# Performance work log

Hardware: AMD Instinct MI355X
Metric: run time of the kernel (lower is better)

Reference implementation:

```python
import jax, jax.numpy as jnp
import numpy as np

B, M, HS, K = 2, 2048, 1024, 16
D = HS // K


def setup_inputs() -> dict:
    key = jax.random.key(0)
    k1, k2, k3, k4 = jax.random.split(key, 4)
    s = 1.0 / np.sqrt(HS)
    return {
        "h": jax.random.normal(k1, (B, M, HS), jnp.float32),
        "W_span": jax.random.normal(k2, (2 * K, HS), jnp.float32) * s,
        "W_val": jax.random.normal(k3, (HS, HS), jnp.float32) * s,
        "W_out": jax.random.normal(k4, (HS, HS), jnp.float32) * s,
    }


def _head_reshape(x, d):
    # (B, M, K*d) -> (B*K, M, d), matching torch view/transpose in head_reshape
    b, m, _ = x.shape
    return x.reshape(b, m, K, d).transpose(0, 2, 1, 3).reshape(b * K, m, d)


def reference(h, W_span, W_val, W_out):
    b, m, hs = h.shape
    span = _head_reshape(h @ W_span.T, 2)        # (B*K, M, 2)
    value = _head_reshape(h @ W_val.T, D)        # (B*K, M, D)
    # AutoSelectAttention: learned per-position Gaussian span over absolute positions
    pos = jnp.arange(m, dtype=h.dtype)           # (M,)
    mean = jax.nn.sigmoid(span[..., 0]) * m      # (B*K, M) span center in [0, M]
    soft = jax.nn.softplus(span[..., 1])         # (B*K, M) sharpness >= 0
    diff = pos[None, None, :] - mean[..., None]  # (B*K, M, M)
    scores = -soft[..., None] * (diff * diff)
    attn = jax.nn.softmax(scores, axis=-1)       # (B*K, M, M)
    out = jnp.matmul(attn, value)                # (B*K, M, D)
    out = out.reshape(b, K, m, D).transpose(0, 2, 1, 3).reshape(b, m, hs)
    return out @ W_out.T
```

## Files before the change

kernel.cpp:

```cpp
#include <hip/hip_runtime.h>
#include <hip/hip_bf16.h>

#define MM   2048
#define HSZ  1024
#define KH   16
#define DH   64

typedef __attribute__((ext_vector_type(8))) short bf16x8;
typedef __attribute__((ext_vector_type(4))) float f32x4;
typedef __attribute__((ext_vector_type(8))) unsigned short u16x8;

#define GLOAD_LDS16(gp, lp) \
    __builtin_amdgcn_global_load_lds( \
        (const __attribute__((address_space(1))) unsigned int*)(gp), \
        (__attribute__((address_space(3))) unsigned int*)(lp), 16, 0, 0)

__device__ __forceinline__ unsigned short f2bf(float x) {
    union { float f; unsigned u; } v; v.f = x;
    unsigned r = v.u + 0x7FFFu + ((v.u >> 16) & 1u);
    return (unsigned short)(r >> 16);
}

__global__ __launch_bounds__(256) void pre_fused(
    const float* __restrict__ h, const float* __restrict__ Wspan,
    const float* __restrict__ Wval, const float* __restrict__ Wout,
    float* __restrict__ mean_, float* __restrict__ soft_,
    unsigned short* __restrict__ h_bf,
    unsigned short* __restrict__ Wval_bf, unsigned short* __restrict__ Wout_bf)
{
    __shared__ float red[4][16][33];
    int t = threadIdx.x;

    if (blockIdx.x >= 256) {
        int bid = blockIdx.x - 256;
        #pragma unroll
        for (int i = 0; i < 4; ++i) {
            int fi = bid * 1024 + i * 256 + t;
            const float* in; unsigned short* out; int off;
            if (fi < 1048576)      { in = h;    out = h_bf;    off = fi; }
            else if (fi < 1310720) { in = Wval; out = Wval_bf; off = fi - 1048576; }
            else                   { in = Wout; out = Wout_bf; off = fi - 1310720; }
            float4 v = *(const float4*)(in + (long)off * 4);
            ushort4 o4;
            o4.x = f2bf(v.x); o4.y = f2bf(v.y); o4.z = f2bf(v.z); o4.w = f2bf(v.w);
            *(ushort4*)(out + (long)off * 4) = o4;
        }
        return;
    }

    int blk = blockIdx.x;
    int wid = t >> 6, l = t & 63;
    int lr = l & 15, lhi = l >> 4;
    int m0 = blk * 16;
    const float* hrow = h + (long)(m0 + lr) * HSZ + wid * 256;

    f32x4 acc[2] = {};

    #define SPLIT8(af_, hh_, hl_) { \
        _Pragma("unroll") for (int j_ = 0; j_ < 8; ++j_) { \
            unsigned short hu_ = f2bf(af_[j_]); \
            union { unsigned u; float f; } cv_; cv_.u = (unsigned)hu_ << 16; \
            hh_[j_] = (short)hu_; hl_[j_] = (short)f2bf(af_[j_] - cv_.f); } }

    #pragma unroll
    for (int ks = 0; ks < 8; ++ks) {
        int k0 = ks * 32 + lhi * 8;
        float4 a0 = *(const float4*)(hrow + k0);
        float4 a1 = *(const float4*)(hrow + k0 + 4);
        float af[8] = {a0.x, a0.y, a0.z, a0.w, a1.x, a1.y, a1.z, a1.w};
        bf16x8 hh, hl;
        SPLIT8(af, hh, hl);
        #pragma unroll
        for (int ct = 0; ct < 2; ++ct) {
            const float* wrow = Wspan + (long)(ct * 16 + lr) * HSZ + wid * 256 + k0;
            float4 w0 = *(const float4*)wrow;
            float4 w1 = *(const float4*)(wrow + 4);
            float wf[8] = {w0.x, w0.y, w0.z, w0.w, w1.x, w1.y, w1.z, w1.w};
            bf16x8 wh, wl;
            SPLIT8(wf, wh, wl);
            acc[ct] = __builtin_amdgcn_mfma_f32_16x16x32_bf16(hh, wh, acc[ct], 0, 0, 0);
            acc[ct] = __builtin_amdgcn_mfma_f32_16x16x32_bf16(hh, wl, acc[ct], 0, 0, 0);
            acc[ct] = __builtin_amdgcn_mfma_f32_16x16x32_bf16(hl, wh, acc[ct], 0, 0, 0);
        }
    }
    #undef SPLIT8

    #pragma unroll
    for (int ct = 0; ct < 2; ++ct)
        #pragma unroll
        for (int r_ = 0; r_ < 4; ++r_)
            red[wid][lhi * 4 + r_][ct * 16 + lr] = acc[ct][r_];
    __syncthreads();

    int r = t >> 4, o2 = t & 15;
    #pragma unroll
    for (int half = 0; half < 2; ++half) {
        int o = half * 16 + o2;
        float s = red[0][r][o] + red[1][r][o] + red[2][r][o] + red[3][r][o];
        int m = m0 + r;
        int bb = m >> 11, mm = m & 2047;
        int bk = bb * KH + (o >> 1);
        if (!(o & 1)) mean_[bk * MM + mm] = (1.f / (1.f + __expf(-s))) * (float)MM;
        else          soft_[bk * MM + mm] = (s > 15.f) ? s : log1pf(__expf(s));
    }
}

#define SROW(li) ((li) >> 3)
#define SCOL(li) ((((li) & 7) ^ (SROW(li) & 7)) * 8)

template<int STORE_BF16>
__device__ __forceinline__ void gemm_core64(
    unsigned short* __restrict__ AsB, unsigned short* __restrict__ BsB,
    const unsigned short* __restrict__ A, const unsigned short* __restrict__ Bm,
    void* __restrict__ Cv, int N, int Kd,
    int bx, int by, int bz, long aZ, long bZ, long cZ)
{
    const unsigned short* Ab = A  + bz * aZ;
    const unsigned short* Bb = Bm + bz * bZ;
    long czoff = bz * cZ;
    int row0 = by * 64;
    int col0 = bx * 64;
    int t = threadIdx.x;
    int wid = t >> 6, l = t & 63;
    int wr = wid >> 1, wc = wid & 1;
    int lr = l & 15, lhi = l >> 4;

    #define STAGE64(buf, k0s) do { \
        unsigned short* As_ = AsB + (buf) * 4096; \
        unsigned short* Bs_ = BsB + (buf) * 4096; \
        int a0 = t, a1 = t + 256; \
        GLOAD_LDS16(Ab + (long)(row0 + SROW(a0)) * Kd + (k0s) + SCOL(a0), As_ + a0 * 8); \
        GLOAD_LDS16(Ab + (long)(row0 + SROW(a1)) * Kd + (k0s) + SCOL(a1), As_ + a1 * 8); \
        GLOAD_LDS16(Bb + (long)(col0 + SROW(a0)) * Kd + (k0s) + SCOL(a0), Bs_ + a0 * 8); \
        GLOAD_LDS16(Bb + (long)(col0 + SROW(a1)) * Kd + (k0s) + SCOL(a1), Bs_ + a1 * 8); \
    } while (0)

    f32x4 acc[2][2] = {};
    int nk = Kd >> 6;

    STAGE64(0, 0);

    for (int ks = 0; ks < nk; ++ks) {
        int cur = ks & 1;
        if (ks + 1 < nk) {
            STAGE64(cur ^ 1, (ks + 1) << 6);
            asm volatile("s_waitcnt vmcnt(4)" ::: "memory");
        } else {
            asm volatile("s_waitcnt vmcnt(0)" ::: "memory");
        }
        __builtin_amdgcn_s_barrier();

        bf16x8 af[2][2], bfr[2][2];
        #pragma unroll
        for (int kk = 0; kk < 2; ++kk) {
            int slotx = ((kk * 4 + lhi) ^ (lr & 7)) << 3;
            #pragma unroll
            for (int i = 0; i < 2; ++i)
                af[kk][i] = *(const bf16x8*)(AsB + cur * 4096 + (wr * 32 + i * 16 + lr) * 64 + slotx);
            #pragma unroll
            for (int j = 0; j < 2; ++j)
                bfr[kk][j] = *(const bf16x8*)(BsB + cur * 4096 + (wc * 32 + j * 16 + lr) * 64 + slotx);
        }
        asm volatile("s_waitcnt lgkmcnt(0)" ::: "memory");
        __builtin_amdgcn_sched_barrier(0);
        __builtin_amdgcn_s_barrier();

        #pragma unroll
        for (int kk = 0; kk < 2; ++kk)
            #pragma unroll
            for (int i = 0; i < 2; ++i)
                #pragma unroll
                for (int j = 0; j < 2; ++j)
                    acc[i][j] = __builtin_amdgcn_mfma_f32_16x16x32_bf16(af[kk][i], bfr[kk][j], acc[i][j], 0, 0, 0);
    }
    #undef STAGE64

    #pragma unroll
    for (int i = 0; i < 2; ++i) {
        int rbase = row0 + wr * 32 + i * 16 + lhi * 4;
        #pragma unroll
        for (int j = 0; j < 2; ++j) {
            int cidx = col0 + wc * 32 + j * 16 + lr;
            #pragma unroll
            for (int r_ = 0; r_ < 4; ++r_) {
                long idx = czoff + (long)(rbase + r_) * N + cidx;
                if (STORE_BF16) ((unsigned short*)Cv)[idx] = f2bf(acc[i][j][r_]);
                else            ((float*)Cv)[idx] = acc[i][j][r_];
            }
        }
    }
}

__device__ void sort_core(char* smem, const float* __restrict__ mean_,
                          int* __restrict__ perm, int bk)
{
    unsigned short (*hist)[257] = (unsigned short(*)[257])smem;
    int* binTot = (int*)(smem + 16448);
    int* binStart = binTot + 32;
    int t = threadIdx.x;
    int bins[8];
    #pragma unroll
    for (int i = 0; i < 8; ++i) {
        float mq = mean_[bk * MM + t * 8 + i];
        int b = (int)(mq * (1.f / 64.f));
        bins[i] = min(31, max(0, b));
    }
    for (int b = 0; b < 32; ++b) hist[b][t] = 0;
    __syncthreads();
    #pragma unroll
    for (int i = 0; i < 8; ++i) hist[bins[i]][t]++;
    __syncthreads();
    int w = t >> 6, l = t & 63;
    for (int b = w * 8; b < w * 8 + 8; ++b) {
        int carry = 0;
        for (int g = 0; g < 4; ++g) {
            int v = (int)hist[b][g * 64 + l];
            int x = v;
            #pragma unroll
            for (int off = 1; off < 64; off <<= 1) {
                int y = __shfl_up(x, off, 64);
                if (l >= off) x += y;
            }
            hist[b][g * 64 + l] = (unsigned short)(x - v + carry);
            carry += __shfl(x, 63, 64);
        }
        if (l == 0) binTot[b] = carry;
    }
    __syncthreads();
    if (t == 0) {
        int s = 0;
        for (int b = 0; b < 32; ++b) { binStart[b] = s; s += binTot[b]; }
    }
    __syncthreads();
    #pragma unroll
    for (int i = 0; i < 8; ++i) {
        int b = bins[i];
        int prior = 0;
        #pragma unroll
        for (int j = 0; j < 8; ++j) if (j < i && bins[j] == b) prior++;
        int pos = binStart[b] + (int)hist[b][t] + prior;
        perm[bk * MM + pos] = t * 8 + i;
    }
}

__global__ __launch_bounds__(256) void vgemm_sort(
    const unsigned short* __restrict__ Wval_bf, const unsigned short* __restrict__ h_bf,
    unsigned short* __restrict__ hvT,
    const float* __restrict__ mean_, int* __restrict__ perm)
{
    __shared__ __align__(16) char smem[32768];
    int f = blockIdx.x;
    if (f < 1024) {
        int swz = (f & 7) * 128 + (f >> 3);
        int by = swz & 15, r = swz >> 4;
        int bx = r & 31, bz = r >> 5;
        gemm_core64<1>((unsigned short*)smem, (unsigned short*)(smem + 16384),
                       Wval_bf, h_bf, hvT, MM, HSZ, bx, by, bz,
                       0L, (long)MM * HSZ, (long)HSZ * MM);
    } else {
        sort_core(smem, mean_, perm, f - 1024);
    }
}

__global__ __launch_bounds__(256) void ogemm(
    const unsigned short* __restrict__ att, const unsigned short* __restrict__ Wout_bf,
    float* __restrict__ out)
{
    __shared__ __align__(16) unsigned short As[2][4096];
    __shared__ __align__(16) unsigned short Bs[2][4096];
    int f = blockIdx.x;
    int swz = (f & 7) * 128 + (f >> 3);
    int bx = swz & 15, by = (swz >> 4) & 63;
    gemm_core64<0>(&As[0][0], &Bs[0][0], att, Wout_bf, out, HSZ, HSZ,
                   bx, by, 0, 0L, 0L, 0L);
}

__global__ __launch_bounds__(512) void attn_gauss(
    const float* __restrict__ mean_, const float* __restrict__ soft_,
    const int* __restrict__ perm,
    const unsigned short* __restrict__ hvT, unsigned short* __restrict__ att)
{
    __shared__ __align__(16) unsigned short Vs[2][64 * 64];
    __shared__ float red[2][8];
    int flat = blockIdx.x;
    int swz = (flat & 7) * 64 + (flat >> 3);
    int bk = swz >> 4;
    int qb = swz & 15;
    int t = threadIdx.x, wid = t >> 6, l = t & 63;
    int b = bk >> 4, head = bk & 15;
    int lr = l & 15, lhi = l >> 4;
    int slot = qb * 128 + wid * 16 + lr;
    int q = perm[bk * MM + slot];
    float mq  = mean_[bk * MM + q];
    float sq  = soft_[bk * MM + q];
    const unsigned short* Vbase = hvT + (long)bk * DH * MM;

    float w = __fsqrt_rn(50.f / sq);
    float lo = mq - w, hi = mq + w;
    #pragma unroll
    for (int off = 1; off < 64; off <<= 1) {
        lo = fminf(lo, __shfl_xor(lo, off, 64));
        hi = fmaxf(hi, __shfl_xor(hi, off, 64));
    }
    if (l == 0) { red[0][wid] = lo; red[1][wid] = hi; }
    __syncthreads();
    float blo = red[0][0], bhi = red[1][0];
    #pragma unroll
    for (int i = 1; i < 8; ++i) {
        blo = fminf(blo, red[0][i]);
        bhi = fmaxf(bhi, red[1][i]);
    }
    blo = fmaxf(blo, 0.f);
    bhi = fmaxf(fminf(bhi, 2047.f), 0.f);
    int kt0 = ((int)blo) >> 6;
    int kt1 = ((int)bhi) >> 6;
    if (kt1 < kt0) kt1 = kt0;

    int sr = t >> 3;
    int sc = (((t & 7) ^ (sr & 7)) * 8);

    f32x4 acc[4] = {};
    float lsum = 0.f;
    int jlane0 = lhi * 8;

    GLOAD_LDS16(Vbase + (long)sr * MM + (kt0 << 6) + sc, &Vs[0][t * 8]);
    __syncthreads();

    for (int kt = kt0; kt <= kt1; ++kt) {
        int cur = (kt - kt0) & 1;
        int k0 = kt << 6;
        if (kt < kt1)
            GLOAD_LDS16(Vbase + (long)sr * MM + (k0 + 64) + sc, &Vs[cur ^ 1][t * 8]);

        float dmin = fmaxf(fmaxf((float)k0 - mq, mq - (float)(k0 + 63)), 0.f);
        bool active = (sq * dmin * dmin) < 50.f;
        if (__ballot(active)) {
            #pragma unroll
            for (int kk = 0; kk < 64; kk += 32) {
                bf16x8 pfrag;
                float dbase = (float)(k0 + kk + jlane0) - mq;
                #pragma unroll
                for (int jj = 0; jj < 8; ++jj) {
                    float d_ = dbase + (float)jj;
                    float p = __expf(-sq * d_ * d_);
                    lsum += p;
                    pfrag[jj] = (short)f2bf(p);
                }
                int slotx = (((kk >> 3) + lhi) ^ (lr & 7)) << 3;
                #pragma unroll
                for (int df = 0; df < 4; ++df) {
                    bf16x8 vf = *(const bf16x8*)&Vs[cur][(df * 16 + lr) * 64 + slotx];
                    acc[df] = __builtin_amdgcn_mfma_f32_16x16x32_bf16(pfrag, vf, acc[df], 0, 0, 0);
                }
            }
        }
        __syncthreads();
    }

    lsum += __shfl_xor(lsum, 16, 64);
    lsum += __shfl_xor(lsum, 32, 64);

    int slot_base = qb * 128 + wid * 16;
    #pragma unroll
    for (int r_ = 0; r_ < 4; ++r_) {
        int qr = lhi * 4 + r_;
        float inv = 1.f / __shfl(lsum, qr, 64);
        int qo = perm[bk * MM + slot_base + qr];
        long orow = ((long)b * MM + qo) * HSZ + head * DH;
        #pragma unroll
        for (int df = 0; df < 4; ++df)
            att[orow + df * 16 + lr] = f2bf(acc[df][r_] * inv);
    }
}

extern "C" void kernel_launch(void* const* d_in, const int* in_sizes, int n_in,
                              void* d_out, int out_size, void* d_ws, size_t ws_size,
                              hipStream_t stream) {
    (void)in_sizes; (void)n_in; (void)out_size; (void)ws_size;
    const float* h     = (const float*)d_in[0];
    const float* Wspan = (const float*)d_in[1];
    const float* Wval  = (const float*)d_in[2];
    const float* Wout  = (const float*)d_in[3];
    float* out = (float*)d_out;

    char* ws = (char*)d_ws;
    unsigned short* h_bf    = (unsigned short*)(ws);
    unsigned short* Wval_bf = (unsigned short*)(ws +  8388608);
    unsigned short* Wout_bf = (unsigned short*)(ws + 10485760);
    unsigned short* hvT     = (unsigned short*)(ws + 12582912);
    unsigned short* att     = (unsigned short*)(ws + 20971520);
    float*          mean_   = (float*)(ws + 29360128);
    float*          soft_   = (float*)(ws + 29622272);
    int*            perm    = (int*)(ws + 29884416);

    pre_fused<<<1792, 256, 0, stream>>>(h, Wspan, Wval, Wout,
                                        mean_, soft_, h_bf, Wval_bf, Wout_bf);

    vgemm_sort<<<1056, 256, 0, stream>>>(Wval_bf, h_bf, hvT, mean_, perm);

    attn_gauss<<<512, 512, 0, stream>>>(mean_, soft_, perm, hvT, att);

    ogemm<<<1024, 256, 0, stream>>>(att, Wout_bf, out);
}
```

Before: 65.96 us.

## Compute per-wave key-tile span and load V directly from global, dropping LDS staging

```diff
diff --git a/kernel.cpp b/kernel.cpp
--- a/kernel.cpp
+++ b/kernel.cpp
@@ -280,8 +280,6 @@
     const int* __restrict__ perm,
     const unsigned short* __restrict__ hvT, unsigned short* __restrict__ att)
 {
-    __shared__ __align__(16) unsigned short Vs[2][64 * 64];
-    __shared__ float red[2][8];
     int flat = blockIdx.x;
     int swz = (flat & 7) * 64 + (flat >> 3);
     int bk = swz >> 4;
@@ -298,63 +296,41 @@
     float w = __fsqrt_rn(50.f / sq);
     float lo = mq - w, hi = mq + w;
     #pragma unroll
-    for (int off = 1; off < 64; off <<= 1) {
+    for (int off = 1; off < 16; off <<= 1) {
         lo = fminf(lo, __shfl_xor(lo, off, 64));
         hi = fmaxf(hi, __shfl_xor(hi, off, 64));
     }
-    if (l == 0) { red[0][wid] = lo; red[1][wid] = hi; }
-    __syncthreads();
-    float blo = red[0][0], bhi = red[1][0];
-    #pragma unroll
-    for (int i = 1; i < 8; ++i) {
-        blo = fminf(blo, red[0][i]);
-        bhi = fmaxf(bhi, red[1][i]);
-    }
-    blo = fmaxf(blo, 0.f);
-    bhi = fmaxf(fminf(bhi, 2047.f), 0.f);
-    int kt0 = ((int)blo) >> 6;
-    int kt1 = ((int)bhi) >> 6;
+    lo = fmaxf(lo, 0.f);
+    hi = fmaxf(fminf(hi, 2047.f), 0.f);
+    int kt0 = ((int)lo) >> 6;
+    int kt1 = ((int)hi) >> 6;
     if (kt1 < kt0) kt1 = kt0;
-
-    int sr = t >> 3;
-    int sc = (((t & 7) ^ (sr & 7)) * 8);
 
     f32x4 acc[4] = {};
     float lsum = 0.f;
     int jlane0 = lhi * 8;
 
-    GLOAD_LDS16(Vbase + (long)sr * MM + (kt0 << 6) + sc, &Vs[0][t * 8]);
-    __syncthreads();
-
     for (int kt = kt0; kt <= kt1; ++kt) {
-        int cur = (kt - kt0) & 1;
         int k0 = kt << 6;
-        if (kt < kt1)
-            GLOAD_LDS16(Vbase + (long)sr * MM + (k0 + 64) + sc, &Vs[cur ^ 1][t * 8]);
-
-        float dmin = fmaxf(fmaxf((float)k0 - mq, mq - (float)(k0 + 63)), 0.f);
-        bool active = (sq * dmin * dmin) < 50.f;
-        if (__ballot(active)) {
-            #pragma unroll
-            for (int kk = 0; kk < 64; kk += 32) {
-                bf16x8 pfrag;
-                float dbase = (float)(k0 + kk + jlane0) - mq;
-                #pragma unroll
-                for (int jj = 0; jj < 8; ++jj) {
-                    float d_ = dbase + (float)jj;
-                    float p = __expf(-sq * d_ * d_);
-                    lsum += p;
-                    pfrag[jj] = (short)f2bf(p);
-                }
-                int slotx = (((kk >> 3) + lhi) ^ (lr & 7)) << 3;
-                #pragma unroll
-                for (int df = 0; df < 4; ++df) {
-                    bf16x8 vf = *(const bf16x8*)&Vs[cur][(df * 16 + lr) * 64 + slotx];
-                    acc[df] = __builtin_amdgcn_mfma_f32_16x16x32_bf16(pfrag, vf, acc[df], 0, 0, 0);
-                }
+        #pragma unroll
+        for (int kk = 0; kk < 64; kk += 32) {
+            bf16x8 vf[4];
+            #pragma unroll
+            for (int df = 0; df < 4; ++df)
+                vf[df] = *(const bf16x8*)(Vbase + (long)(df * 16 + lr) * MM + k0 + kk + jlane0);
+            bf16x8 pfrag;
+            float dbase = (float)(k0 + kk + jlane0) - mq;
+            #pragma unroll
+            for (int jj = 0; jj < 8; ++jj) {
+                float d_ = dbase + (float)jj;
+                float p = __expf(-sq * d_ * d_);
+                lsum += p;
+                pfrag[jj] = (short)f2bf(p);
             }
-        }
-        __syncthreads();
+            #pragma unroll
+            for (int df = 0; df < 4; ++df)
+                acc[df] = __builtin_amdgcn_mfma_f32_16x16x32_bf16(pfrag, vf[df], acc[df], 0, 0, 0);
+        }
     }
 
     lsum += __shfl_xor(lsum, 16, 64);
```

Result: slower. 70.25 us (+6.5%).
